# Optimization experiments

Measured on AMD Instinct MI355X. Metric: run time of the kernel, lower is better.

Reference implementation:

```python
import jax, jax.numpy as jnp
import numpy as np

N = 32768      # total points (8 clouds x 4096)
B = 8          # clouds in batch
D_IN = 64      # input feature dim
M = 8192       # sampled centers (ratio=0.25)
K = 32         # knn neighbors
R = 0.2        # ball radius
DIMS = [D_IN + 3, 128, 128, 256]  # edge MLP (PointNetConv local_nn)


def setup_inputs() -> dict:
    key = jax.random.key(0)
    ks = jax.random.split(key, 10)
    x = jax.random.normal(ks[0], (N, D_IN), jnp.float32)
    pos = jax.random.uniform(ks[1], (N, 3), jnp.float32)  # unit cube
    batch = jnp.repeat(jnp.arange(B, dtype=jnp.int32), N // B)
    # deterministic stand-in for torch.sort(torch.randperm(N)[:M])
    idx = jnp.sort(jax.random.permutation(ks[2], N)[:M]).astype(jnp.int32)
    params = {}
    for i in range(3):
        fan_in = DIMS[i]
        params[f"W{i+1}"] = jax.random.normal(ks[3 + 2 * i], (DIMS[i], DIMS[i + 1]), jnp.float32) / np.sqrt(fan_in)
        params[f"b{i+1}"] = jnp.zeros((DIMS[i + 1],), jnp.float32)
    return {"x": x, "pos": pos, "batch": batch, "idx": idx, **params}


def _knn_ball(pos, batch, idx, k, r):
    """Batched KNN restricted to same cloud, then radius mask (ball query)."""
    centers = pos[idx]                                   # [M, 3]
    d2 = (jnp.sum(centers ** 2, -1)[:, None]
          + jnp.sum(pos ** 2, -1)[None, :]
          - 2.0 * centers @ pos.T)                       # [M, N]
    same = batch[idx][:, None] == batch[None, :]
    d2 = jnp.where(same, d2, jnp.inf)
    neg_d2, nbr = jax.lax.top_k(-d2, k)                  # [M, K]
    valid = (-neg_d2) <= r * r                           # ball-query radius clip
    return nbr, valid


def reference(x, pos, batch, idx, W1, b1, W2, b2, W3, b3):
    nbr, valid = _knn_ball(pos, batch, idx, K, R)        # [M,K], [M,K]
    centers = pos[idx]                                   # [M, 3]
    rel = pos[nbr] - centers[:, None, :]                 # [M, K, 3]
    feat = jnp.concatenate([x[nbr], rel], axis=-1)       # [M, K, D_IN+3]
    h = jax.nn.relu(feat @ W1 + b1)
    h = jax.nn.relu(h @ W2 + b2)
    h = jax.nn.relu(h @ W3 + b3)                         # [M, K, 256]
    # max aggregation over valid neighbors (scatter-max equivalent)
    h = jnp.where(valid[:, :, None], h, -jnp.inf)
    out = jnp.max(h, axis=1)                             # [M, 256]
    return out, pos[idx], batch[idx]
```

## Files before the change

kernel.cpp:

```cpp
#include <hip/hip_runtime.h>


typedef unsigned short u16;
typedef unsigned int u32;
typedef unsigned long long u64;
typedef __bf16 bf16x8 __attribute__((ext_vector_type(8)));
typedef float floatx4 __attribute__((ext_vector_type(4)));

#define PCLOUD 4096
#define DIN    64
#define MCENT  8192
#define KNBR   32
#define CAP    448

#define OFF_LIST  0
#define OFF_HIST  14336
#define OFF_NBRL  14848
#define OFF_CNT   15360
#define OFF_CEN   15392
#define OFF_BCL   15456

__device__ inline u16 f2bf(float f) {
    u32 b = __float_as_uint(f);
    b += 0x7fffu + ((b >> 16) & 1u);
    return (u16)(b >> 16);
}
__device__ inline u32 cvtpk(float a, float b) {
    u32 r;
    asm("v_cvt_pk_bf16_f32 %0, %1, %2" : "=v"(r) : "v"(a), "v"(b));
    return r;
}
__device__ inline u64 wave_min_u64(u64 v) {
    #pragma unroll
    for (int off = 32; off; off >>= 1) {
        u64 o = __shfl_xor((unsigned long long)v, off);
        if (o < v) v = o;
    }
    return v;
}
__device__ inline u64 d2key(float d2, int j) {
    u32 u = __float_as_uint(d2);
    u = (u & 0x80000000u) ? ~u : (u | 0x80000000u);
    return ((u64)u << 32) | (u32)j;
}
__device__ inline int key_bucket(u64 k) {
    u32 hi = (u32)(k >> 32);
    if (hi < 0x80000000u) return 0;
    float d2 = __uint_as_float(hi & 0x7fffffffu);
    int b = (int)(d2 * 800.0f);
    return b > 31 ? 31 : b;
}

__global__ void prep_kernel(const float* __restrict__ W1, const float* __restrict__ W2,
                            const float* __restrict__ W3, uint4* __restrict__ ws) {
    int t = blockIdx.x * 256 + threadIdx.x;
    int g = t >> 11, r = t & 2047;
    int n = r >> 4, kc = r & 15;
    const float* W; int rs, n0, krows;
    if (g == 0)      { W = W1; rs = 128; n0 = 0;   krows = 67;  }
    else if (g == 1) { W = W2; rs = 128; n0 = 0;   krows = 128; }
    else if (g == 2) { W = W3; rs = 256; n0 = 0;   krows = 128; }
    else             { W = W3; rs = 256; n0 = 128; krows = 128; }
    u16 e[8];
    #pragma unroll
    for (int j = 0; j < 8; j++) {
        int k = kc * 8 + j;
        e[j] = (k < krows) ? f2bf(W[(size_t)k * rs + n0 + n]) : (u16)0;
    }
    ws[(g << 11) + (n << 4) + (kc ^ (n & 7))] = *(const uint4*)e;
}

__device__ __forceinline__ uint4 ldB_ws(const uint4* __restrict__ ws4, int blk, int cb, int m16) {
    return ws4[blk * 256 + (m16 << 4) + (cb ^ (m16 & 7))];
}
__device__ __forceinline__ uint4 ldB_fb(const float* __restrict__ W, int rs, int col,
                                        int cb, int krows) {
    u16 e[8];
    #pragma unroll
    for (int j = 0; j < 8; j++) {
        int k = cb * 8 + j;
        e[j] = (k < krows) ? f2bf(W[(size_t)k * rs + col]) : (u16)0;
    }
    return *(const uint4*)e;
}

__device__ __forceinline__ void push_hit(int c, float d2, int j,
                                         int* acnt, u64* lists) {
    int p = atomicAdd(&acnt[c], 1);
    if (p < CAP) lists[c * CAP + p] = d2key(d2, j);
}

template <bool WS>
__global__ __launch_bounds__(256, 4) void sa_kernel(
    const float* __restrict__ x, const float* __restrict__ pos,
    const int* __restrict__ batch, const int* __restrict__ idx,
    const float* __restrict__ W1, const float* __restrict__ b1,
    const float* __restrict__ W2, const float* __restrict__ b2,
    const float* __restrict__ W3, const float* __restrict__ b3,
    const uint4* __restrict__ ws4, float* __restrict__ out) {
    __shared__ __align__(16) char smem[32768];
    u64*  lists = (u64*)(smem + OFF_LIST);
    u32*  hist  = (u32*)(smem + OFF_HIST);
    int*  nbrl  = (int*)(smem + OFF_NBRL);
    int*  acnt  = (int*)(smem + OFF_CNT);
    int*  cnt2  = (int*)(smem + OFF_CNT + 16);
    float4* cen = (float4*)(smem + OFF_CEN);
    int*  bcls  = (int*)(smem + OFF_BCL);
    uint4* sA4  = (uint4*)smem;

    int tid = threadIdx.x, w = tid >> 6, l = tid & 63;
    int bid = blockIdx.x;
    int m0 = ((bid & 7) << 10) + ((bid >> 3) << 2);
    int m = m0 + w;
    int ic = idx[m] & (8 * PCLOUD - 1);
    float cx = pos[ic * 3], cy = pos[ic * 3 + 1], cz = pos[ic * 3 + 2];
    float sc = __fadd_rn(__fadd_rn(__fmul_rn(cx, cx), __fmul_rn(cy, cy)), __fmul_rn(cz, cz));
    int bcl = batch[ic] & 7;
    int base = bcl << 12;
    const float R2 = 0.04f;

    if (l == 0) { cen[w] = make_float4(cx, cy, cz, sc); bcls[w] = bcl; }
    if (tid < 4) { acnt[tid] = 0; cnt2[tid] = 0; }
    if (l == 1) {
        float* o1 = out + MCENT * 256;
        o1[m * 3] = cx; o1[m * 3 + 1] = cy; o1[m * 3 + 2] = cz;
        (o1 + MCENT * 3)[m] = (float)bcl;
    }
    __syncthreads();

    bool uni = (bcls[0] == bcls[1]) && (bcls[1] == bcls[2]) && (bcls[2] == bcls[3]);
    if (uni) {
        float4 cA = cen[0], cB = cen[1], cC = cen[2], cD = cen[3];
        int jb = bcls[0] << 12;
        const float4* pb4 = (const float4*)(pos + (size_t)jb * 3);

#define TEST1(CEN, CI, SP, PX, PY, PZ, J) { \
    float dt = __fadd_rn(__fadd_rn(__fmul_rn(CEN.x, PX), __fmul_rn(CEN.y, PY)), __fmul_rn(CEN.z, PZ)); \
    float d2 = __fsub_rn(__fadd_rn(CEN.w, SP), __fmul_rn(2.0f, dt)); \
    if (d2 <= R2) push_hit(CI, d2, J, acnt, lists); }
#define TESTP(PX, PY, PZ, J) { \
    float sp = __fadd_rn(__fadd_rn(__fmul_rn(PX, PX), __fmul_rn(PY, PY)), __fmul_rn(PZ, PZ)); \
    TEST1(cA, 0, sp, PX, PY, PZ, J) \
    TEST1(cB, 1, sp, PX, PY, PZ, J) \
    TEST1(cC, 2, sp, PX, PY, PZ, J) \
    TEST1(cD, 3, sp, PX, PY, PZ, J) }

        #pragma unroll
        for (int it = 0; it < 4; it++) {
            int tq = it * 256 + tid;
            float4 q0 = pb4[tq * 3], q1 = pb4[tq * 3 + 1], q2 = pb4[tq * 3 + 2];
            int j0 = jb + tq * 4;
            TESTP(q0.x, q0.y, q0.z, j0)
            TESTP(q0.w, q1.x, q1.y, j0 + 1)
            TESTP(q1.z, q1.w, q2.x, j0 + 2)
            TESTP(q2.y, q2.z, q2.w, j0 + 3)
        }
#undef TESTP
#undef TEST1
    } else {
        for (int t = l; t < PCLOUD; t += 64) {
            int j = base + t;
            float px = pos[j * 3], py = pos[j * 3 + 1], pz = pos[j * 3 + 2];
            float sp = __fadd_rn(__fadd_rn(__fmul_rn(px, px), __fmul_rn(py, py)), __fmul_rn(pz, pz));
            float dt = __fadd_rn(__fadd_rn(__fmul_rn(cx, px), __fmul_rn(cy, py)), __fmul_rn(cz, pz));
            float d2 = __fsub_rn(__fadd_rn(sc, sp), __fmul_rn(2.0f, dt));
            if (d2 <= R2) push_hit(w, d2, j, acnt, lists);
        }
    }
    __syncthreads();

    int c = acnt[w];
    int nsel = c < KNBR ? c : KNBR;
    u64* mylist = lists + w * CAP;

    int selj = -1;
    if (c <= KNBR) {
        if (l < c) selj = (int)(u32)mylist[l];
    } else if (c <= CAP) {
        u64 kk[7];
        int bk[7];
        if (l < 32) hist[w * 32 + l] = 0;
        #pragma unroll
        for (int i = 0; i < 7; i++) kk[i] = (l + i * 64 < c) ? mylist[l + i * 64] : ~0ull;
        #pragma unroll
        for (int i = 0; i < 7; i++) {
            bk[i] = 32;
            if (kk[i] != ~0ull) {
                bk[i] = key_bucket(kk[i]);
                atomicAdd(&hist[w * 32 + bk[i]], 1u);
            }
        }
        int hv = (l < 32) ? (int)hist[w * 32 + l] : 0;
        #pragma unroll
        for (int off = 1; off <= 16; off <<= 1) {
            int o = __shfl_up(hv, off);
            if (l >= off) hv += o;
        }
        u64 ge = __ballot((l < 32) && (hv >= KNBR));
        int B = __ffsll((unsigned long long)ge) - 1;
        int S = (B == 0) ? 0 : __shfl(hv, B - 1);
        #pragma unroll
        for (int i = 0; i < 7; i++) {
            if (kk[i] != ~0ull) {
                if (bk[i] < B) { int p = atomicAdd(&cnt2[w], 1); nbrl[w * 32 + p] = (int)(u32)kk[i]; }
                if (bk[i] != B) kk[i] = ~0ull;
            }
        }
        int need = KNBR - S;
        u64 last = 0;
        for (int r = 0; r < need; r++) {
            u64 mn = ~0ull;
            #pragma unroll
            for (int i = 0; i < 7; i++) if (kk[i] > last && kk[i] < mn) mn = kk[i];
            mn = wave_min_u64(mn);
            if (l == 0) nbrl[w * 32 + S + r] = (int)(u32)mn;
            last = mn;
        }
        if (l < KNBR) selj = nbrl[w * 32 + l];
    } else {
        u64 last = 0;
        for (int r = 0; r < KNBR; r++) {
            u64 mn = ~0ull;
            for (int t = l; t < PCLOUD; t += 64) {
                int j = base + t;
                float px = pos[j * 3], py = pos[j * 3 + 1], pz = pos[j * 3 + 2];
                float sp = __fadd_rn(__fadd_rn(__fmul_rn(px, px), __fmul_rn(py, py)), __fmul_rn(pz, pz));
                float dt = __fadd_rn(__fadd_rn(__fmul_rn(cx, px), __fmul_rn(cy, py)), __fmul_rn(cz, pz));
                float d2 = __fsub_rn(__fadd_rn(sc, sp), __fmul_rn(2.0f, dt));
                if (d2 <= R2) { u64 kf = d2key(d2, j); if (kf > last && kf < mn) mn = kf; }
            }
            mn = wave_min_u64(mn);
            if (l == r) selj = (int)(u32)mn;
            last = mn;
        }
    }
    __syncthreads();

    {
        int h = l & 1, rl = l >> 1;
        int row = w * 32 + rl;
        int j = __shfl(selj, rl);
        int xv = row & 7;
        uint4* dst = sA4 + row * 16;
        uint4 z; z.x = z.y = z.z = z.w = 0;
        if (j >= 0) {
            const float4* sx = (const float4*)(x + (size_t)j * DIN);
            int c0lo = h ? 6 : 0, c0hi = h ? 8 : 6;
            for (int c0 = c0lo; c0 < c0hi; c0++) {
                float4 f0 = sx[c0 * 2], f1 = sx[c0 * 2 + 1];
                uint4 pv;
                pv.x = cvtpk(f0.x, f0.y); pv.y = cvtpk(f0.z, f0.w);
                pv.z = cvtpk(f1.x, f1.y); pv.w = cvtpk(f1.z, f1.w);
                dst[c0 ^ xv] = pv;
            }
            if (h == 1) {
                float rx = pos[j * 3] - cx, ry = pos[j * 3 + 1] - cy, rz = pos[j * 3 + 2] - cz;
                uint4 rc; rc.x = cvtpk(rx, ry); rc.y = cvtpk(rz, 0.0f); rc.z = 0; rc.w = 0;
                dst[8 ^ xv] = rc;
                dst[9 ^ xv] = z; dst[10 ^ xv] = z; dst[11 ^ xv] = z;
            }
        } else {
            int c0lo = h ? 6 : 0, c0hi = h ? 12 : 6;
            for (int c0 = c0lo; c0 < c0hi; c0++) dst[c0 ^ xv] = z;
        }
    }

    int m16 = l & 15, quad = l >> 4;
    int r0 = w * 32;
    const floatx4 vzero = {0.f, 0.f, 0.f, 0.f};

#define LDB(BLK, CB, W, RS, COL, KR) \
    (WS ? ldB_ws(ws4, (BLK), (CB), m16) : ldB_fb((W), (RS), (COL), (CB), (KR)))

    {
        bf16x8 a1[3][2];
        #pragma unroll
        for (int ki = 0; ki < 3; ki++)
            #pragma unroll
            for (int t = 0; t < 2; t++) {
                int row = r0 + t * 16 + m16;
                a1[ki][t] = __builtin_bit_cast(bf16x8, sA4[row * 16 + ((ki * 4 + quad) ^ (row & 7))]);
            }
        uint4 bc[3];
        #pragma unroll
        for (int ki = 0; ki < 3; ki++) bc[ki] = LDB(0, ki * 4 + quad, W1, 128, m16, 67);
        #pragma unroll
        for (int s = 0; s < 8; s++) {
            uint4 bn[3];
            if (s < 7) {
                #pragma unroll
                for (int ki = 0; ki < 3; ki++)
                    bn[ki] = LDB(s + 1, ki * 4 + quad, W1, 128, (s + 1) * 16 + m16, 67);
            }
            floatx4 acc[2] = {vzero, vzero};
            __builtin_amdgcn_s_setprio(1);
            #pragma unroll
            for (int ki = 0; ki < 3; ki++) {
                bf16x8 b = __builtin_bit_cast(bf16x8, bc[ki]);
                #pragma unroll
                for (int t = 0; t < 2; t++)
                    acc[t] = __builtin_amdgcn_mfma_f32_16x16x32_bf16(b, a1[ki][t], acc[t], 0, 0, 0);
            }
            __builtin_amdgcn_s_setprio(0);
            float4 bb = ((const float4*)b1)[s * 4 + quad];
            #pragma unroll
            for (int t = 0; t < 2; t++) {
                int rr = r0 + t * 16 + m16;
                uint2 pv;
                pv.x = cvtpk(fmaxf(acc[t][0] + bb.x, 0.f), fmaxf(acc[t][1] + bb.y, 0.f));
                pv.y = cvtpk(fmaxf(acc[t][2] + bb.z, 0.f), fmaxf(acc[t][3] + bb.w, 0.f));
                *(uint2*)(smem + rr * 256 + (((s * 2 + (quad >> 1)) ^ (rr & 7)) << 4) + ((quad & 1) << 3)) = pv;
            }
            if (s < 7) {
                #pragma unroll
                for (int ki = 0; ki < 3; ki++) bc[ki] = bn[ki];
            }
        }
    }

    {
        bf16x8 a2[4][2];
        #pragma unroll
        for (int ki = 0; ki < 4; ki++)
            #pragma unroll
            for (int t = 0; t < 2; t++) {
                int row = r0 + t * 16 + m16;
                a2[ki][t] = __builtin_bit_cast(bf16x8, sA4[row * 16 + ((ki * 4 + quad) ^ (row & 7))]);
            }
        uint4 bc[4];
        #pragma unroll
        for (int ki = 0; ki < 4; ki++) bc[ki] = LDB(8, ki * 4 + quad, W2, 128, m16, 128);
        #pragma unroll
        for (int s = 0; s < 8; s++) {
            uint4 bn[4];
            if (s < 7) {
                #pragma unroll
                for (int ki = 0; ki < 4; ki++)
                    bn[ki] = LDB(9 + s, ki * 4 + quad, W2, 128, (s + 1) * 16 + m16, 128);
            }
            floatx4 acc[2] = {vzero, vzero};
            __builtin_amdgcn_s_setprio(1);
            #pragma unroll
            for (int ki = 0; ki < 4; ki++) {
                bf16x8 b = __builtin_bit_cast(bf16x8, bc[ki]);
                #pragma unroll
                for (int t = 0; t < 2; t++)
                    acc[t] = __builtin_amdgcn_mfma_f32_16x16x32_bf16(b, a2[ki][t], acc[t], 0, 0, 0);
            }
            __builtin_amdgcn_s_setprio(0);
            float4 bb = ((const float4*)b2)[s * 4 + quad];
            #pragma unroll
            for (int t = 0; t < 2; t++) {
                int rr = r0 + t * 16 + m16;
                uint2 pv;
                pv.x = cvtpk(fmaxf(acc[t][0] + bb.x, 0.f), fmaxf(acc[t][1] + bb.y, 0.f));
                pv.y = cvtpk(fmaxf(acc[t][2] + bb.z, 0.f), fmaxf(acc[t][3] + bb.w, 0.f));
                *(uint2*)(smem + rr * 256 + (((s * 2 + (quad >> 1)) ^ (rr & 7)) << 4) + ((quad & 1) << 3)) = pv;
            }
            if (s < 7) {
                #pragma unroll
                for (int ki = 0; ki < 4; ki++) bc[ki] = bn[ki];
            }
        }
    }

    {
        bf16x8 a3[4][2];
        #pragma unroll
        for (int ki = 0; ki < 4; ki++)
            #pragma unroll
            for (int t = 0; t < 2; t++) {
                int row = r0 + t * 16 + m16;
                a3[ki][t] = __builtin_bit_cast(bf16x8, sA4[row * 16 + ((ki * 4 + quad) ^ (row & 7))]);
            }
        uint4 bc[4];
        #pragma unroll
        for (int ki = 0; ki < 4; ki++) bc[ki] = LDB(16, ki * 4 + quad, W3, 256, m16, 128);
        #pragma unroll
        for (int s = 0; s < 16; s++) {
            uint4 bn[4];
            if (s < 15) {
                #pragma unroll
                for (int ki = 0; ki < 4; ki++)
                    bn[ki] = LDB(17 + s, ki * 4 + quad, W3, 256, (s + 1) * 16 + m16, 128);
            }
            floatx4 acc[2] = {vzero, vzero};
            __builtin_amdgcn_s_setprio(1);
            #pragma unroll
            for (int ki = 0; ki < 4; ki++) {
                bf16x8 b = __builtin_bit_cast(bf16x8, bc[ki]);
                #pragma unroll
                for (int t = 0; t < 2; t++)
                    acc[t] = __builtin_amdgcn_mfma_f32_16x16x32_bf16(a3[ki][t], b, acc[t], 0, 0, 0);
            }
            __builtin_amdgcn_s_setprio(0);
            int col = s * 16 + m16;
            float bias = b3[col];
            float mv = 0.0f;
            #pragma unroll
            for (int t = 0; t < 2; t++)
                #pragma unroll
                for (int i = 0; i < 4; i++) {
                    int k = t * 16 + quad * 4 + i;
                    float v = fmaxf(acc[t][i] + bias, 0.0f);
                    if (k < nsel) mv = fmaxf(mv, v);
                }
            mv = fmaxf(mv, __shfl_xor(mv, 16));
            mv = fmaxf(mv, __shfl_xor(mv, 32));
            if (quad == 0) out[(m0 + w) * 256 + col] = mv;
            if (s < 15) {
                #pragma unroll
                for (int ki = 0; ki < 4; ki++) bc[ki] = bn[ki];
            }
        }
    }
#undef LDB
}

extern "C" void kernel_launch(void* const* d_in, const int* in_sizes, int n_in,
                              void* d_out, int out_size, void* d_ws, size_t ws_size,
                              hipStream_t stream) {
    const float* x     = (const float*)d_in[0];
    const float* pos   = (const float*)d_in[1];
    const int*   batch = (const int*)d_in[2];
    const int*   idx   = (const int*)d_in[3];
    const float* W1    = (const float*)d_in[4];
    const float* b1    = (const float*)d_in[5];
    const float* W2    = (const float*)d_in[6];
    const float* b2    = (const float*)d_in[7];
    const float* W3    = (const float*)d_in[8];
    const float* b3    = (const float*)d_in[9];
    float* out = (float*)d_out;
    uint4* ws4 = (uint4*)d_ws;

    if (ws_size >= 131072) {
        hipLaunchKernelGGL(prep_kernel, dim3(32), dim3(256), 0, stream, W1, W2, W3, ws4);
        hipLaunchKernelGGL((sa_kernel<true>), dim3(MCENT / 4), dim3(256), 0, stream,
                           x, pos, batch, idx, W1, b1, W2, b2, W3, b3, ws4, out);
    } else {
        hipLaunchKernelGGL((sa_kernel<false>), dim3(MCENT / 4), dim3(256), 0, stream,
                           x, pos, batch, idx, W1, b1, W2, b2, W3, b3, ws4, out);
    }
}
```

Baseline: 163.7 us.

## Double-buffer MLP weight prefetch, batch gather loads, rebalance distance histogram buckets

Each of the three MLP layers now keeps two register buffers of B-operand weights and prefetches two column blocks ahead, issuing the next loads after the MFMAs rather than before. The aim is to hide more global/L2 weight-load latency behind the matrix math. The neighbor feature gather is unrolled so all float4 loads for a row are issued together before conversion, exposing memory-level parallelism. The distance histogram bucket function switches from linear in d2 to proportional to d2^1.5, which roughly tracks neighbor counts in a uniform ball. This spreads candidates more evenly across buckets for the kNN selection, at the cost of extra registers and a sqrt per key.

```diff
diff --git a/kernel.cpp b/kernel.cpp
--- a/kernel.cpp
+++ b/kernel.cpp
@@ -47,8 +47,10 @@
     u32 hi = (u32)(k >> 32);
     if (hi < 0x80000000u) return 0;
     float d2 = __uint_as_float(hi & 0x7fffffffu);
-    int b = (int)(d2 * 800.0f);
-    return b > 31 ? 31 : b;
+    float t = d2 * 25.0f;
+    float b = 32.0f * t * __builtin_sqrtf(t);
+    int bi = (int)b;
+    return bi > 31 ? 31 : (bi < 0 ? 0 : bi);
 }
 
 __global__ void prep_kernel(const float* __restrict__ W1, const float* __restrict__ W2,
@@ -245,23 +247,45 @@
         uint4 z; z.x = z.y = z.z = z.w = 0;
         if (j >= 0) {
             const float4* sx = (const float4*)(x + (size_t)j * DIN);
-            int c0lo = h ? 6 : 0, c0hi = h ? 8 : 6;
-            for (int c0 = c0lo; c0 < c0hi; c0++) {
-                float4 f0 = sx[c0 * 2], f1 = sx[c0 * 2 + 1];
-                uint4 pv;
-                pv.x = cvtpk(f0.x, f0.y); pv.y = cvtpk(f0.z, f0.w);
-                pv.z = cvtpk(f1.x, f1.y); pv.w = cvtpk(f1.z, f1.w);
-                dst[c0 ^ xv] = pv;
-            }
-            if (h == 1) {
+            if (h == 0) {
+                float4 f[12];
+                #pragma unroll
+                for (int i = 0; i < 12; i++) f[i] = sx[i];
+                #pragma unroll
+                for (int c0 = 0; c0 < 6; c0++) {
+                    uint4 pv;
+                    pv.x = cvtpk(f[c0 * 2].x, f[c0 * 2].y);
+                    pv.y = cvtpk(f[c0 * 2].z, f[c0 * 2].w);
+                    pv.z = cvtpk(f[c0 * 2 + 1].x, f[c0 * 2 + 1].y);
+                    pv.w = cvtpk(f[c0 * 2 + 1].z, f[c0 * 2 + 1].w);
+                    dst[c0 ^ xv] = pv;
+                }
+            } else {
+                float4 f[4];
+                #pragma unroll
+                for (int i = 0; i < 4; i++) f[i] = sx[12 + i];
                 float rx = pos[j * 3] - cx, ry = pos[j * 3 + 1] - cy, rz = pos[j * 3 + 2] - cz;
+                #pragma unroll
+                for (int c0 = 0; c0 < 2; c0++) {
+                    uint4 pv;
+                    pv.x = cvtpk(f[c0 * 2].x, f[c0 * 2].y);
+                    pv.y = cvtpk(f[c0 * 2].z, f[c0 * 2].w);
+                    pv.z = cvtpk(f[c0 * 2 + 1].x, f[c0 * 2 + 1].y);
+                    pv.w = cvtpk(f[c0 * 2 + 1].z, f[c0 * 2 + 1].w);
+                    dst[(6 + c0) ^ xv] = pv;
+                }
                 uint4 rc; rc.x = cvtpk(rx, ry); rc.y = cvtpk(rz, 0.0f); rc.z = 0; rc.w = 0;
                 dst[8 ^ xv] = rc;
                 dst[9 ^ xv] = z; dst[10 ^ xv] = z; dst[11 ^ xv] = z;
             }
         } else {
-            int c0lo = h ? 6 : 0, c0hi = h ? 12 : 6;
-            for (int c0 = c0lo; c0 < c0hi; c0++) dst[c0 ^ xv] = z;
+            if (h == 0) {
+                #pragma unroll
+                for (int c0 = 0; c0 < 6; c0++) dst[c0 ^ xv] = z;
+            } else {
+                #pragma unroll
+                for (int c0 = 6; c0 < 12; c0++) dst[c0 ^ xv] = z;
+            }
         }
     }
 
@@ -271,6 +295,17 @@
 
 #define LDB(BLK, CB, W, RS, COL, KR) \
     (WS ? ldB_ws(ws4, (BLK), (CB), m16) : ldB_fb((W), (RS), (COL), (CB), (KR)))
+
+#define EPI12(BPTR, S, ACC) { \
+    float4 bb = ((const float4*)(BPTR))[(S) * 4 + quad]; \
+    _Pragma("unroll") \
+    for (int t = 0; t < 2; t++) { \
+        int rr = r0 + t * 16 + m16; \
+        uint2 pv; \
+        pv.x = cvtpk(fmaxf(ACC[t][0] + bb.x, 0.f), fmaxf(ACC[t][1] + bb.y, 0.f)); \
+        pv.y = cvtpk(fmaxf(ACC[t][2] + bb.z, 0.f), fmaxf(ACC[t][3] + bb.w, 0.f)); \
+        *(uint2*)(smem + rr * 256 + ((((S) * 2 + (quad >> 1)) ^ (rr & 7)) << 4) + ((quad & 1) << 3)) = pv; \
+    } }
 
     {
         bf16x8 a1[3][2];
@@ -281,39 +316,48 @@
                 int row = r0 + t * 16 + m16;
                 a1[ki][t] = __builtin_bit_cast(bf16x8, sA4[row * 16 + ((ki * 4 + quad) ^ (row & 7))]);
             }
-        uint4 bc[3];
-        #pragma unroll
-        for (int ki = 0; ki < 3; ki++) bc[ki] = LDB(0, ki * 4 + quad, W1, 128, m16, 67);
-        #pragma unroll
-        for (int s = 0; s < 8; s++) {
-            uint4 bn[3];
-            if (s < 7) {
-                #pragma unroll
-                for (int ki = 0; ki < 3; ki++)
-                    bn[ki] = LDB(s + 1, ki * 4 + quad, W1, 128, (s + 1) * 16 + m16, 67);
-            }
-            floatx4 acc[2] = {vzero, vzero};
-            __builtin_amdgcn_s_setprio(1);
-            #pragma unroll
-            for (int ki = 0; ki < 3; ki++) {
-                bf16x8 b = __builtin_bit_cast(bf16x8, bc[ki]);
-                #pragma unroll
-                for (int t = 0; t < 2; t++)
-                    acc[t] = __builtin_amdgcn_mfma_f32_16x16x32_bf16(b, a1[ki][t], acc[t], 0, 0, 0);
-            }
-            __builtin_amdgcn_s_setprio(0);
-            float4 bb = ((const float4*)b1)[s * 4 + quad];
-            #pragma unroll
-            for (int t = 0; t < 2; t++) {
-                int rr = r0 + t * 16 + m16;
-                uint2 pv;
-                pv.x = cvtpk(fmaxf(acc[t][0] + bb.x, 0.f), fmaxf(acc[t][1] + bb.y, 0.f));
-                pv.y = cvtpk(fmaxf(acc[t][2] + bb.z, 0.f), fmaxf(acc[t][3] + bb.w, 0.f));
-                *(uint2*)(smem + rr * 256 + (((s * 2 + (quad >> 1)) ^ (rr & 7)) << 4) + ((quad & 1) << 3)) = pv;
-            }
-            if (s < 7) {
-                #pragma unroll
-                for (int ki = 0; ki < 3; ki++) bc[ki] = bn[ki];
+        uint4 p0[3], p1[3];
+        #pragma unroll
+        for (int ki = 0; ki < 3; ki++) p0[ki] = LDB(0, ki * 4 + quad, W1, 128, m16, 67);
+        #pragma unroll
+        for (int ki = 0; ki < 3; ki++) p1[ki] = LDB(1, ki * 4 + quad, W1, 128, 16 + m16, 67);
+        #pragma unroll
+        for (int s = 0; s < 8; s += 2) {
+            {
+                floatx4 acc[2] = {vzero, vzero};
+                __builtin_amdgcn_s_setprio(1);
+                #pragma unroll
+                for (int ki = 0; ki < 3; ki++) {
+                    bf16x8 b = __builtin_bit_cast(bf16x8, p0[ki]);
+                    #pragma unroll
+                    for (int t = 0; t < 2; t++)
+                        acc[t] = __builtin_amdgcn_mfma_f32_16x16x32_bf16(b, a1[ki][t], acc[t], 0, 0, 0);
+                }
+                __builtin_amdgcn_s_setprio(0);
+                if (s + 2 < 8) {
+                    #pragma unroll
+                    for (int ki = 0; ki < 3; ki++)
+                        p0[ki] = LDB(s + 2, ki * 4 + quad, W1, 128, (s + 2) * 16 + m16, 67);
+                }
+                EPI12(b1, s, acc);
+            }
+            {
+                floatx4 acc[2] = {vzero, vzero};
+                __builtin_amdgcn_s_setprio(1);
+                #pragma unroll
+                for (int ki = 0; ki < 3; ki++) {
+                    bf16x8 b = __builtin_bit_cast(bf16x8, p1[ki]);
+                    #pragma unroll
+                    for (int t = 0; t < 2; t++)
+                        acc[t] = __builtin_amdgcn_mfma_f32_16x16x32_bf16(b, a1[ki][t], acc[t], 0, 0, 0);
+                }
+                __builtin_amdgcn_s_setprio(0);
+                if (s + 3 < 8) {
+                    #pragma unroll
+                    for (int ki = 0; ki < 3; ki++)
+                        p1[ki] = LDB(s + 3, ki * 4 + quad, W1, 128, (s + 3) * 16 + m16, 67);
+                }
+                EPI12(b1, s + 1, acc);
             }
         }
     }
@@ -327,42 +371,67 @@
                 int row = r0 + t * 16 + m16;
                 a2[ki][t] = __builtin_bit_cast(bf16x8, sA4[row * 16 + ((ki * 4 + quad) ^ (row & 7))]);
             }
-        uint4 bc[4];
-        #pragma unroll
-        for (int ki = 0; ki < 4; ki++) bc[ki] = LDB(8, ki * 4 + quad, W2, 128, m16, 128);
-        #pragma unroll
-        for (int s = 0; s < 8; s++) {
-            uint4 bn[4];
-            if (s < 7) {
-                #pragma unroll
-                for (int ki = 0; ki < 4; ki++)
-                    bn[ki] = LDB(9 + s, ki * 4 + quad, W2, 128, (s + 1) * 16 + m16, 128);
-            }
-            floatx4 acc[2] = {vzero, vzero};
-            __builtin_amdgcn_s_setprio(1);
-            #pragma unroll
-            for (int ki = 0; ki < 4; ki++) {
-                bf16x8 b = __builtin_bit_cast(bf16x8, bc[ki]);
-                #pragma unroll
-                for (int t = 0; t < 2; t++)
-                    acc[t] = __builtin_amdgcn_mfma_f32_16x16x32_bf16(b, a2[ki][t], acc[t], 0, 0, 0);
-            }
-            __builtin_amdgcn_s_setprio(0);
-            float4 bb = ((const float4*)b2)[s * 4 + quad];
-            #pragma unroll
-            for (int t = 0; t < 2; t++) {
-                int rr = r0 + t * 16 + m16;
-                uint2 pv;
-                pv.x = cvtpk(fmaxf(acc[t][0] + bb.x, 0.f), fmaxf(acc[t][1] + bb.y, 0.f));
-                pv.y = cvtpk(fmaxf(acc[t][2] + bb.z, 0.f), fmaxf(acc[t][3] + bb.w, 0.f));
-                *(uint2*)(smem + rr * 256 + (((s * 2 + (quad >> 1)) ^ (rr & 7)) << 4) + ((quad & 1) << 3)) = pv;
-            }
-            if (s < 7) {
-                #pragma unroll
-                for (int ki = 0; ki < 4; ki++) bc[ki] = bn[ki];
-            }
-        }
-    }
+        uint4 p0[4], p1[4];
+        #pragma unroll
+        for (int ki = 0; ki < 4; ki++) p0[ki] = LDB(8, ki * 4 + quad, W2, 128, m16, 128);
+        #pragma unroll
+        for (int ki = 0; ki < 4; ki++) p1[ki] = LDB(9, ki * 4 + quad, W2, 128, 16 + m16, 128);
+        #pragma unroll
+        for (int s = 0; s < 8; s += 2) {
+            {
+                floatx4 acc[2] = {vzero, vzero};
+                __builtin_amdgcn_s_setprio(1);
+                #pragma unroll
+                for (int ki = 0; ki < 4; ki++) {
+                    bf16x8 b = __builtin_bit_cast(bf16x8, p0[ki]);
+                    #pragma unroll
+                    for (int t = 0; t < 2; t++)
+                        acc[t] = __builtin_amdgcn_mfma_f32_16x16x32_bf16(b, a2[ki][t], acc[t], 0, 0, 0);
+                }
+                __builtin_amdgcn_s_setprio(0);
+                if (s + 2 < 8) {
+                    #pragma unroll
+                    for (int ki = 0; ki < 4; ki++)
+                        p0[ki] = LDB(8 + s + 2, ki * 4 + quad, W2, 128, (s + 2) * 16 + m16, 128);
+                }
+                EPI12(b2, s, acc);
+            }
+            {
+                floatx4 acc[2] = {vzero, vzero};
+                __builtin_amdgcn_s_setprio(1);
+                #pragma unroll
+                for (int ki = 0; ki < 4; ki++) {
+                    bf16x8 b = __builtin_bit_cast(bf16x8, p1[ki]);
+                    #pragma unroll
+                    for (int t = 0; t < 2; t++)
+                        acc[t] = __builtin_amdgcn_mfma_f32_16x16x32_bf16(b, a2[ki][t], acc[t], 0, 0, 0);
+                }
+                __builtin_amdgcn_s_setprio(0);
+                if (s + 3 < 8) {
+                    #pragma unroll
+                    for (int ki = 0; ki < 4; ki++)
+                        p1[ki] = LDB(8 + s + 3, ki * 4 + quad, W2, 128, (s + 3) * 16 + m16, 128);
+                }
+                EPI12(b2, s + 1, acc);
+            }
+        }
+    }
+
+#define EPI3(S, ACC) { \
+    int col = (S) * 16 + m16; \
+    float bias = b3[col]; \
+    float mv = 0.0f; \
+    _Pragma("unroll") \
+    for (int t = 0; t < 2; t++) \
+        _Pragma("unroll") \
+        for (int i = 0; i < 4; i++) { \
+            int k = t * 16 + quad * 4 + i; \
+            float v = fmaxf(ACC[t][i] + bias, 0.0f); \
+            if (k < nsel) mv = fmaxf(mv, v); \
+        } \
+    mv = fmaxf(mv, __shfl_xor(mv, 16)); \
+    mv = fmaxf(mv, __shfl_xor(mv, 32)); \
+    if (quad == 0) out[(m0 + w) * 256 + col] = mv; }
 
     {
         bf16x8 a3[4][2];
@@ -373,48 +442,54 @@
                 int row = r0 + t * 16 + m16;
                 a3[ki][t] = __builtin_bit_cast(bf16x8, sA4[row * 16 + ((ki * 4 + quad) ^ (row & 7))]);
             }
-        uint4 bc[4];
-        #pragma unroll
-        for (int ki = 0; ki < 4; ki++) bc[ki] = LDB(16, ki * 4 + quad, W3, 256, m16, 128);
-        #pragma unroll
-        for (int s = 0; s < 16; s++) {
-            uint4 bn[4];
-            if (s < 15) {
-                #pragma unroll
-                for (int ki = 0; ki < 4; ki++)
-                    bn[ki] = LDB(17 + s, ki * 4 + quad, W3, 256, (s + 1) * 16 + m16, 128);
-            }
-            floatx4 acc[2] = {vzero, vzero};
-            __builtin_amdgcn_s_setprio(1);
-            #pragma unroll
-            for (int ki = 0; ki < 4; ki++) {
-                bf16x8 b = __builtin_bit_cast(bf16x8, bc[ki]);
-                #pragma unroll
-                for (int t = 0; t < 2; t++)
-                    acc[t] = __builtin_amdgcn_mfma_f32_16x16x32_bf16(a3[ki][t], b, acc[t], 0, 0, 0);
-            }
-            __builtin_amdgcn_s_setprio(0);
-            int col = s * 16 + m16;
-            float bias = b3[col];
-            float mv = 0.0f;
-            #pragma unroll
-            for (int t = 0; t < 2; t++)
-                #pragma unroll
-                for (int i = 0; i < 4; i++) {
-                    int k = t * 16 + quad * 4 + i;
-                    float v = fmaxf(acc[t][i] + bias, 0.0f);
-                    if (k < nsel) mv = fmaxf(mv, v);
-                }
-            mv = fmaxf(mv, __shfl_xor(mv, 16));
-            mv = fmaxf(mv, __shfl_xor(mv, 32));
-            if (quad == 0) out[(m0 + w) * 256 + col] = mv;
-            if (s < 15) {
-                #pragma unroll
-                for (int ki = 0; ki < 4; ki++) bc[ki] = bn[ki];
+        uint4 p0[4], p1[4];
+        #pragma unroll
+        for (int ki = 0; ki < 4; ki++) p0[ki] = LDB(16, ki * 4 + quad, W3, 256, m16, 128);
+        #pragma unroll
+        for (int ki = 0; ki < 4; ki++) p1[ki] = LDB(17, ki * 4 + quad, W3, 256, 16 + m16, 128);
+        #pragma unroll
+        for (int s = 0; s < 16; s += 2) {
+            {
+                floatx4 acc[2] = {vzero, vzero};
+                __builtin_amdgcn_s_setprio(1);
+                #pragma unroll
+                for (int ki = 0; ki < 4; ki++) {
+                    bf16x8 b = __builtin_bit_cast(bf16x8, p0[ki]);
+                    #pragma unroll
+                    for (int t = 0; t < 2; t++)
+                        acc[t] = __builtin_amdgcn_mfma_f32_16x16x32_bf16(a3[ki][t], b, acc[t], 0, 0, 0);
+                }
+                __builtin_amdgcn_s_setprio(0);
+                if (s + 2 < 16) {
+                    #pragma unroll
+                    for (int ki = 0; ki < 4; ki++)
+                        p0[ki] = LDB(16 + s + 2, ki * 4 + quad, W3, 256, (s + 2) * 16 + m16, 128);
+                }
+                EPI3(s, acc);
+            }
+            {
+                floatx4 acc[2] = {vzero, vzero};
+                __builtin_amdgcn_s_setprio(1);
+                #pragma unroll
+                for (int ki = 0; ki < 4; ki++) {
+                    bf16x8 b = __builtin_bit_cast(bf16x8, p1[ki]);
+                    #pragma unroll
+                    for (int t = 0; t < 2; t++)
+                        acc[t] = __builtin_amdgcn_mfma_f32_16x16x32_bf16(a3[ki][t], b, acc[t], 0, 0, 0);
+                }
+                __builtin_amdgcn_s_setprio(0);
+                if (s + 3 < 16) {
+                    #pragma unroll
+                    for (int ki = 0; ki < 4; ki++)
+                        p1[ki] = LDB(16 + s + 3, ki * 4 + quad, W3, 256, (s + 3) * 16 + m16, 128);
+                }
+                EPI3(s + 1, acc);
             }
         }
     }
 #undef LDB
+#undef EPI12
+#undef EPI3
 }
 
 extern "C" void kernel_launch(void* const* d_in, const int* in_sizes, int n_in,
```

Result: no change. 162.3 us (-0.9%).
